# Performance work log

Measured on AMD Instinct MI355X. Metric: run time of the kernel, lower is better.

The kernel has to match this reference:

```python
import jax, jax.numpy as jnp
import numpy as np

B, S, T, D = 32, 128, 65536, 768
VOCAB, N_SEC, N_TEMP, N_NEG, MAX_SENT, N_TS = 30522, 6, 3, 2, 128, 512
LN_EPS = 1e-5


def setup_inputs() -> dict:
    key = jax.random.key(0)
    ks = jax.random.split(key, 16)
    return {
        "token_ids": jax.random.randint(ks[0], (T,), 0, VOCAB),
        "segment_ids": jnp.sort(jax.random.randint(ks[1], (T,), 0, B * S)),
        "section_ids": jax.random.randint(ks[2], (B, S), 0, N_SEC),
        "temporality_ids": jax.random.randint(ks[3], (B, S), 0, N_TEMP),
        "negation_ids": jax.random.randint(ks[4], (B, S), 0, N_NEG),
        "position_ids": jax.random.randint(ks[5], (B, S), 0, MAX_SENT),
        "timestamp_ids": jax.random.randint(ks[6], (B, S), 0, N_TS),
        "token_table": jax.random.normal(ks[7], (VOCAB, D), jnp.float32),
        "section_table": jax.random.normal(ks[8], (N_SEC, D), jnp.float32),
        "temporality_table": jax.random.normal(ks[9], (N_TEMP, D), jnp.float32),
        "negation_table": jax.random.normal(ks[10], (N_NEG, D), jnp.float32),
        "position_table": jax.random.normal(ks[11], (MAX_SENT, D), jnp.float32),
        "timestamp_table": jax.random.normal(ks[12], (N_TS, D), jnp.float32),
        "ln_gamma": jnp.ones((D,), jnp.float32),
        "ln_beta": jnp.zeros((D,), jnp.float32),
        "proj_w": jax.random.normal(ks[13], (D, D), jnp.float32) * (1.0 / np.sqrt(D)),
        "proj_b": jnp.zeros((D,), jnp.float32),
    }


def reference(token_ids, segment_ids, section_ids, temporality_ids, negation_ids,
              position_ids, timestamp_ids, token_table, section_table,
              temporality_table, negation_table, position_table, timestamp_table,
              ln_gamma, ln_beta, proj_w, proj_b):
    # ragged per-sentence token-embedding mean pool (segment mean over B*S slots)
    tok = token_table[token_ids]                                  # [T, D]
    sums = jax.ops.segment_sum(tok, segment_ids, num_segments=B * S)
    cnt = jax.ops.segment_sum(jnp.ones((T,), tok.dtype), segment_ids,
                              num_segments=B * S)
    base = (sums / jnp.maximum(cnt, 1.0)[:, None]).reshape(B, S, D)
    # multi-embedding sum
    enriched = (base
                + section_table[section_ids]
                + temporality_table[temporality_ids]
                + negation_table[negation_ids]
                + position_table[position_ids]
                + timestamp_table[timestamp_ids])                 # [B, S, D]
    # LayerNorm + Linear
    mu = enriched.mean(-1, keepdims=True)
    var = jnp.mean(jnp.square(enriched - mu), axis=-1, keepdims=True)
    normed = (enriched - mu) * jax.lax.rsqrt(var + LN_EPS) * ln_gamma + ln_beta
    tokens = jnp.einsum('bsd,ed->bse', normed, proj_w) + proj_b   # [B, S, D]
    padding_mask = jnp.zeros((B, S), dtype=bool)                  # all sentences valid
    return tokens, padding_mask
```

## Files before the change

### kernel.cpp

```cpp
#include <hip/hip_runtime.h>
#include <stdint.h>

#define Tn 65536
#define Dn 768
#define NSEG 4096

typedef __bf16 bf16;
typedef __bf16 bf16x8 __attribute__((ext_vector_type(8)));
typedef float f32x4 __attribute__((ext_vector_type(4)));

__device__ inline void f4add(float4& a, const float4& v) {
  a.x += v.x; a.y += v.y; a.z += v.z; a.w += v.w;
}

__device__ inline float block_sum192(float v, float* sm) {
  #pragma unroll
  for (int o = 32; o > 0; o >>= 1) v += __shfl_down(v, o, 64);
  const int lane = threadIdx.x & 63, w = threadIdx.x >> 6;
  __syncthreads();
  if (lane == 0) sm[w] = v;
  __syncthreads();
  return sm[0] + sm[1] + sm[2];
}

__global__ __launch_bounds__(192) void k_pool_ln(
    const int* __restrict__ token_ids, const int* __restrict__ segment_ids,
    const int* __restrict__ section_ids, const int* __restrict__ temporality_ids,
    const int* __restrict__ negation_ids, const int* __restrict__ position_ids,
    const int* __restrict__ timestamp_ids,
    const float* __restrict__ token_table, const float* __restrict__ section_table,
    const float* __restrict__ temporality_table, const float* __restrict__ negation_table,
    const float* __restrict__ position_table, const float* __restrict__ timestamp_table,
    const float* __restrict__ gamma, const float* __restrict__ beta,
    bf16* __restrict__ out_normed)
{
  const int n = blockIdx.x;
  const int tid = threadIdx.x;
  __shared__ float red[3];

  int lo = 0, hi = Tn;
  while (lo < hi) { int mid = (lo + hi) >> 1; if (segment_ids[mid] < n) lo = mid + 1; else hi = mid; }
  const int start = lo;
  hi = Tn;
  while (lo < hi) { int mid = (lo + hi) >> 1; if (segment_ids[mid] < n + 1) lo = mid + 1; else hi = mid; }
  const int end = lo;
  const float scale = 1.0f / fmaxf((float)(end - start), 1.0f);

  const int sec = section_ids[n];
  const int tmp = temporality_ids[n];
  const int neg = negation_ids[n];
  const int pos = position_ids[n];
  const int ts  = timestamp_ids[n];
  const float4 v1 = *(const float4*)(section_table     + (size_t)sec * Dn + 4 * tid);
  const float4 v2 = *(const float4*)(temporality_table + (size_t)tmp * Dn + 4 * tid);
  const float4 v3 = *(const float4*)(negation_table    + (size_t)neg * Dn + 4 * tid);
  const float4 v4 = *(const float4*)(position_table    + (size_t)pos * Dn + 4 * tid);
  const float4 v5 = *(const float4*)(timestamp_table   + (size_t)ts  * Dn + 4 * tid);

  const float4* tt = (const float4*)token_table;
  float4 a0 = make_float4(0.f,0.f,0.f,0.f), a1 = a0, a2 = a0, a3 = a0;
  int t = start;
  for (; t + 4 <= end; t += 4) {
    const int i0 = token_ids[t + 0];
    const int i1 = token_ids[t + 1];
    const int i2 = token_ids[t + 2];
    const int i3 = token_ids[t + 3];
    const float4 w0 = tt[(size_t)i0 * 192 + tid];
    const float4 w1 = tt[(size_t)i1 * 192 + tid];
    const float4 w2 = tt[(size_t)i2 * 192 + tid];
    const float4 w3 = tt[(size_t)i3 * 192 + tid];
    f4add(a0, w0); f4add(a1, w1); f4add(a2, w2); f4add(a3, w3);
  }
  for (; t < end; ++t) {
    const float4 w0 = tt[(size_t)token_ids[t] * 192 + tid];
    f4add(a0, w0);
  }
  f4add(a0, a1); f4add(a2, a3); f4add(a0, a2);

  float4 e;
  e.x = a0.x * scale + v1.x + v2.x + v3.x + v4.x + v5.x;
  e.y = a0.y * scale + v1.y + v2.y + v3.y + v4.y + v5.y;
  e.z = a0.z * scale + v1.z + v2.z + v3.z + v4.z + v5.z;
  e.w = a0.w * scale + v1.w + v2.w + v3.w + v4.w + v5.w;

  const float mu = block_sum192(e.x + e.y + e.z + e.w, red) * (1.0f / 768.0f);
  const float dx = e.x - mu, dy = e.y - mu, dz = e.z - mu, dw = e.w - mu;
  const float var = block_sum192(dx*dx + dy*dy + dz*dz + dw*dw, red) * (1.0f / 768.0f);
  const float inv = rsqrtf(var + 1e-5f);

  const float4 g = *(const float4*)(gamma + 4 * tid);
  const float4 b = *(const float4*)(beta  + 4 * tid);
  alignas(8) bf16 o[4];
  o[0] = (bf16)(dx * inv * g.x + b.x);
  o[1] = (bf16)(dy * inv * g.y + b.y);
  o[2] = (bf16)(dz * inv * g.z + b.z);
  o[3] = (bf16)(dw * inv * g.w + b.w);
  *(ushort4*)(out_normed + (size_t)n * Dn + 4 * tid) = *(ushort4*)o;
}

__global__ __launch_bounds__(256) void k_cvt_mask(const float* __restrict__ w,
                                                  bf16* __restrict__ wb,
                                                  float* __restrict__ mask_out) {
  const int b = blockIdx.x;
  if (b < 576) {
    const int i = b * 256 + threadIdx.x;
    const float4 v = ((const float4*)w)[i];
    alignas(8) bf16 o[4] = {(bf16)v.x, (bf16)v.y, (bf16)v.z, (bf16)v.w};
    ((ushort4*)wb)[i] = *(ushort4*)o;
  } else {
    mask_out[(b - 576) * 256 + threadIdx.x] = 0.0f;
  }
}

__global__ __launch_bounds__(256) void k_gemm(
    const bf16* __restrict__ A, const bf16* __restrict__ W,
    const float* __restrict__ bias, float* __restrict__ out)
{
  __shared__ bf16 As[64 * 32];
  __shared__ bf16 Bs[128 * 32];
  const int tid  = threadIdx.x;
  const int lane = tid & 63;
  const int w    = tid >> 6;
  const int m0 = blockIdx.y * 64;
  const int n0 = blockIdx.x * 128;
  const int wm = (w >> 1) * 32;
  const int wn = (w & 1) * 64;

  f32x4 acc[2][4];
  #pragma unroll
  for (int i = 0; i < 2; ++i)
    #pragma unroll
    for (int j = 0; j < 4; ++j) acc[i][j] = (f32x4){0.f, 0.f, 0.f, 0.f};

  const int fr = tid >> 2;
  const int fc = (tid & 3) * 8;
  const bf16* agp = A + (size_t)(m0 + fr) * 768 + fc;
  const bf16* bgp = W + (size_t)(n0 + fr) * 768 + fc;

  for (int kt = 0; kt < 24; ++kt) {
    __syncthreads();
    __builtin_amdgcn_global_load_lds(
        (const __attribute__((address_space(1))) void*)(agp + kt * 32),
        (__attribute__((address_space(3))) void*)(As + tid * 8), 16, 0, 0);
    #pragma unroll
    for (int it = 0; it < 2; ++it) {
      const int f = it * 256 + tid;
      __builtin_amdgcn_global_load_lds(
          (const __attribute__((address_space(1))) void*)(bgp + (size_t)it * 64 * 768 + kt * 32),
          (__attribute__((address_space(3))) void*)(Bs + f * 8), 16, 0, 0);
    }
    __syncthreads();

    bf16x8 af[2], bfr[4];
    #pragma unroll
    for (int i = 0; i < 2; ++i)
      af[i] = *(const bf16x8*)(As + (wm + i * 16 + (lane & 15)) * 32 + (lane >> 4) * 8);
    #pragma unroll
    for (int j = 0; j < 4; ++j)
      bfr[j] = *(const bf16x8*)(Bs + (wn + j * 16 + (lane & 15)) * 32 + (lane >> 4) * 8);

    #pragma unroll
    for (int i = 0; i < 2; ++i)
      #pragma unroll
      for (int j = 0; j < 4; ++j)
        acc[i][j] = __builtin_amdgcn_mfma_f32_16x16x32_bf16(af[i], bfr[j], acc[i][j], 0, 0, 0);
  }

  float bvals[4];
  #pragma unroll
  for (int j = 0; j < 4; ++j) bvals[j] = bias[n0 + wn + j * 16 + (lane & 15)];
  const int r0 = (lane >> 4) * 4;
  #pragma unroll
  for (int i = 0; i < 2; ++i) {
    #pragma unroll
    for (int r = 0; r < 4; ++r) {
      const int gm = m0 + wm + i * 16 + r0 + r;
      float* orow = out + (size_t)gm * 768 + n0 + wn;
      #pragma unroll
      for (int j = 0; j < 4; ++j)
        orow[j * 16 + (lane & 15)] = acc[i][j][r] + bvals[j];
    }
  }
}

extern "C" void kernel_launch(void* const* d_in, const int* in_sizes, int n_in,
                              void* d_out, int out_size, void* d_ws, size_t ws_size,
                              hipStream_t stream) {
  const int* token_ids       = (const int*)d_in[0];
  const int* segment_ids     = (const int*)d_in[1];
  const int* section_ids     = (const int*)d_in[2];
  const int* temporality_ids = (const int*)d_in[3];
  const int* negation_ids    = (const int*)d_in[4];
  const int* position_ids    = (const int*)d_in[5];
  const int* timestamp_ids   = (const int*)d_in[6];
  const float* token_table       = (const float*)d_in[7];
  const float* section_table     = (const float*)d_in[8];
  const float* temporality_table = (const float*)d_in[9];
  const float* negation_table    = (const float*)d_in[10];
  const float* position_table    = (const float*)d_in[11];
  const float* timestamp_table   = (const float*)d_in[12];
  const float* ln_gamma = (const float*)d_in[13];
  const float* ln_beta  = (const float*)d_in[14];
  const float* proj_w   = (const float*)d_in[15];
  const float* proj_b   = (const float*)d_in[16];

  float* out = (float*)d_out;
  bf16* wsW = (bf16*)d_ws;
  bf16* wsN = (bf16*)d_ws + (size_t)Dn * Dn;

  k_cvt_mask<<<592, 256, 0, stream>>>(proj_w, wsW, out + (size_t)NSEG * Dn);
  k_pool_ln<<<NSEG, 192, 0, stream>>>(token_ids, segment_ids, section_ids,
      temporality_ids, negation_ids, position_ids, timestamp_ids,
      token_table, section_table, temporality_table, negation_table,
      position_table, timestamp_table, ln_gamma, ln_beta, wsN);
  k_gemm<<<dim3(6, 64), 256, 0, stream>>>(wsN, wsW, proj_b, out);
}
```

Before: 209.3 us.

## Precompute segment starts and use one wave per segment for pooling+LayerNorm

```diff
diff --git a/kernel.cpp b/kernel.cpp
--- a/kernel.cpp
+++ b/kernel.cpp
@@ -13,18 +13,31 @@
   a.x += v.x; a.y += v.y; a.z += v.z; a.w += v.w;
 }
 
-__device__ inline float block_sum192(float v, float* sm) {
-  #pragma unroll
-  for (int o = 32; o > 0; o >>= 1) v += __shfl_down(v, o, 64);
-  const int lane = threadIdx.x & 63, w = threadIdx.x >> 6;
-  __syncthreads();
-  if (lane == 0) sm[w] = v;
-  __syncthreads();
-  return sm[0] + sm[1] + sm[2];
-}
-
-__global__ __launch_bounds__(192) void k_pool_ln(
-    const int* __restrict__ token_ids, const int* __restrict__ segment_ids,
+__global__ __launch_bounds__(256) void k_prep(
+    const float* __restrict__ w, bf16* __restrict__ wb,
+    float* __restrict__ mask_out,
+    const int* __restrict__ seg, int* __restrict__ starts)
+{
+  const int b = blockIdx.x;
+  if (b < 576) {
+    const int i = b * 256 + threadIdx.x;
+    const float4 v = ((const float4*)w)[i];
+    alignas(8) bf16 o[4] = {(bf16)v.x, (bf16)v.y, (bf16)v.z, (bf16)v.w};
+    ((ushort4*)wb)[i] = *(ushort4*)o;
+  } else if (b < 592) {
+    mask_out[(b - 576) * 256 + threadIdx.x] = 0.0f;
+  } else {
+    const int t = (b - 592) * 256 + threadIdx.x;
+    const int s = seg[t];
+    const int sp = (t == 0) ? -1 : seg[t - 1];
+    for (int k = sp + 1; k <= s; ++k) starts[k] = t;
+    if (t == Tn - 1)
+      for (int k = s + 1; k <= NSEG; ++k) starts[k] = Tn;
+  }
+}
+
+__global__ __launch_bounds__(64) void k_pool_ln(
+    const int* __restrict__ token_ids, const int* __restrict__ starts,
     const int* __restrict__ section_ids, const int* __restrict__ temporality_ids,
     const int* __restrict__ negation_ids, const int* __restrict__ position_ids,
     const int* __restrict__ timestamp_ids,
@@ -35,80 +48,95 @@
     bf16* __restrict__ out_normed)
 {
   const int n = blockIdx.x;
-  const int tid = threadIdx.x;
-  __shared__ float red[3];
-
-  int lo = 0, hi = Tn;
-  while (lo < hi) { int mid = (lo + hi) >> 1; if (segment_ids[mid] < n) lo = mid + 1; else hi = mid; }
-  const int start = lo;
-  hi = Tn;
-  while (lo < hi) { int mid = (lo + hi) >> 1; if (segment_ids[mid] < n + 1) lo = mid + 1; else hi = mid; }
-  const int end = lo;
+  const int lane = threadIdx.x;
+  const int start = starts[n];
+  const int end   = starts[n + 1];
   const float scale = 1.0f / fmaxf((float)(end - start), 1.0f);
 
-  const int sec = section_ids[n];
-  const int tmp = temporality_ids[n];
-  const int neg = negation_ids[n];
-  const int pos = position_ids[n];
-  const int ts  = timestamp_ids[n];
-  const float4 v1 = *(const float4*)(section_table     + (size_t)sec * Dn + 4 * tid);
-  const float4 v2 = *(const float4*)(temporality_table + (size_t)tmp * Dn + 4 * tid);
-  const float4 v3 = *(const float4*)(negation_table    + (size_t)neg * Dn + 4 * tid);
-  const float4 v4 = *(const float4*)(position_table    + (size_t)pos * Dn + 4 * tid);
-  const float4 v5 = *(const float4*)(timestamp_table   + (size_t)ts  * Dn + 4 * tid);
-
   const float4* tt = (const float4*)token_table;
-  float4 a0 = make_float4(0.f,0.f,0.f,0.f), a1 = a0, a2 = a0, a3 = a0;
+
+  const float4* e1 = (const float4*)(section_table     + (size_t)section_ids[n]     * Dn);
+  const float4* e2 = (const float4*)(temporality_table + (size_t)temporality_ids[n] * Dn);
+  const float4* e3 = (const float4*)(negation_table    + (size_t)negation_ids[n]    * Dn);
+  const float4* e4 = (const float4*)(position_table    + (size_t)position_ids[n]    * Dn);
+  const float4* e5 = (const float4*)(timestamp_table   + (size_t)timestamp_ids[n]   * Dn);
+  float4 en[3];
+  #pragma unroll
+  for (int j = 0; j < 3; ++j) {
+    const int d = j * 64 + lane;
+    float4 q = e1[d];
+    f4add(q, e2[d]); f4add(q, e3[d]); f4add(q, e4[d]); f4add(q, e5[d]);
+    en[j] = q;
+  }
+
+  float4 acc[3];
+  #pragma unroll
+  for (int j = 0; j < 3; ++j) acc[j] = make_float4(0.f, 0.f, 0.f, 0.f);
   int t = start;
   for (; t + 4 <= end; t += 4) {
     const int i0 = token_ids[t + 0];
     const int i1 = token_ids[t + 1];
     const int i2 = token_ids[t + 2];
     const int i3 = token_ids[t + 3];
-    const float4 w0 = tt[(size_t)i0 * 192 + tid];
-    const float4 w1 = tt[(size_t)i1 * 192 + tid];
-    const float4 w2 = tt[(size_t)i2 * 192 + tid];
-    const float4 w3 = tt[(size_t)i3 * 192 + tid];
-    f4add(a0, w0); f4add(a1, w1); f4add(a2, w2); f4add(a3, w3);
+    const float4* r0 = tt + (size_t)i0 * 192;
+    const float4* r1 = tt + (size_t)i1 * 192;
+    const float4* r2 = tt + (size_t)i2 * 192;
+    const float4* r3 = tt + (size_t)i3 * 192;
+    float4 L[4][3];
+    #pragma unroll
+    for (int j = 0; j < 3; ++j) {
+      const int d = j * 64 + lane;
+      L[0][j] = r0[d]; L[1][j] = r1[d]; L[2][j] = r2[d]; L[3][j] = r3[d];
+    }
+    #pragma unroll
+    for (int j = 0; j < 3; ++j) {
+      f4add(L[0][j], L[1][j]); f4add(L[2][j], L[3][j]);
+      f4add(L[0][j], L[2][j]); f4add(acc[j], L[0][j]);
+    }
   }
   for (; t < end; ++t) {
-    const float4 w0 = tt[(size_t)token_ids[t] * 192 + tid];
-    f4add(a0, w0);
-  }
-  f4add(a0, a1); f4add(a2, a3); f4add(a0, a2);
-
-  float4 e;
-  e.x = a0.x * scale + v1.x + v2.x + v3.x + v4.x + v5.x;
-  e.y = a0.y * scale + v1.y + v2.y + v3.y + v4.y + v5.y;
-  e.z = a0.z * scale + v1.z + v2.z + v3.z + v4.z + v5.z;
-  e.w = a0.w * scale + v1.w + v2.w + v3.w + v4.w + v5.w;
-
-  const float mu = block_sum192(e.x + e.y + e.z + e.w, red) * (1.0f / 768.0f);
-  const float dx = e.x - mu, dy = e.y - mu, dz = e.z - mu, dw = e.w - mu;
-  const float var = block_sum192(dx*dx + dy*dy + dz*dz + dw*dw, red) * (1.0f / 768.0f);
-  const float inv = rsqrtf(var + 1e-5f);
-
-  const float4 g = *(const float4*)(gamma + 4 * tid);
-  const float4 b = *(const float4*)(beta  + 4 * tid);
-  alignas(8) bf16 o[4];
-  o[0] = (bf16)(dx * inv * g.x + b.x);
-  o[1] = (bf16)(dy * inv * g.y + b.y);
-  o[2] = (bf16)(dz * inv * g.z + b.z);
-  o[3] = (bf16)(dw * inv * g.w + b.w);
-  *(ushort4*)(out_normed + (size_t)n * Dn + 4 * tid) = *(ushort4*)o;
-}
-
-__global__ __launch_bounds__(256) void k_cvt_mask(const float* __restrict__ w,
-                                                  bf16* __restrict__ wb,
-                                                  float* __restrict__ mask_out) {
-  const int b = blockIdx.x;
-  if (b < 576) {
-    const int i = b * 256 + threadIdx.x;
-    const float4 v = ((const float4*)w)[i];
-    alignas(8) bf16 o[4] = {(bf16)v.x, (bf16)v.y, (bf16)v.z, (bf16)v.w};
-    ((ushort4*)wb)[i] = *(ushort4*)o;
-  } else {
-    mask_out[(b - 576) * 256 + threadIdx.x] = 0.0f;
+    const float4* r = tt + (size_t)token_ids[t] * 192;
+    #pragma unroll
+    for (int j = 0; j < 3; ++j) f4add(acc[j], r[j * 64 + lane]);
+  }
+
+  float4 e[3];
+  #pragma unroll
+  for (int j = 0; j < 3; ++j) {
+    e[j].x = acc[j].x * scale + en[j].x;
+    e[j].y = acc[j].y * scale + en[j].y;
+    e[j].z = acc[j].z * scale + en[j].z;
+    e[j].w = acc[j].w * scale + en[j].w;
+  }
+
+  float s = 0.f;
+  #pragma unroll
+  for (int j = 0; j < 3; ++j) s += e[j].x + e[j].y + e[j].z + e[j].w;
+  #pragma unroll
+  for (int o = 32; o > 0; o >>= 1) s += __shfl_xor(s, o, 64);
+  const float mu = s * (1.0f / 768.0f);
+
+  float v = 0.f;
+  #pragma unroll
+  for (int j = 0; j < 3; ++j) {
+    e[j].x -= mu; e[j].y -= mu; e[j].z -= mu; e[j].w -= mu;
+    v += e[j].x * e[j].x + e[j].y * e[j].y + e[j].z * e[j].z + e[j].w * e[j].w;
+  }
+  #pragma unroll
+  for (int o = 32; o > 0; o >>= 1) v += __shfl_xor(v, o, 64);
+  const float inv = rsqrtf(v * (1.0f / 768.0f) + 1e-5f);
+
+  #pragma unroll
+  for (int j = 0; j < 3; ++j) {
+    const int d = j * 64 + lane;
+    const float4 g = ((const float4*)gamma)[d];
+    const float4 b = ((const float4*)beta)[d];
+    alignas(8) bf16 o[4];
+    o[0] = (bf16)(e[j].x * inv * g.x + b.x);
+    o[1] = (bf16)(e[j].y * inv * g.y + b.y);
+    o[2] = (bf16)(e[j].z * inv * g.z + b.z);
+    o[3] = (bf16)(e[j].w * inv * g.w + b.w);
+    *(ushort4*)(out_normed + (size_t)n * Dn + 4 * d) = *(ushort4*)o;
   }
 }
 
@@ -206,10 +234,12 @@
 
   float* out = (float*)d_out;
   bf16* wsW = (bf16*)d_ws;
-  bf16* wsN = (bf16*)d_ws + (size_t)Dn * Dn;
-
-  k_cvt_mask<<<592, 256, 0, stream>>>(proj_w, wsW, out + (size_t)NSEG * Dn);
-  k_pool_ln<<<NSEG, 192, 0, stream>>>(token_ids, segment_ids, section_ids,
+  bf16* wsN = wsW + (size_t)Dn * Dn;
+  int*  wsS = (int*)((char*)d_ws + (size_t)(Dn * Dn + NSEG * Dn) * 2);
+
+  k_prep<<<848, 256, 0, stream>>>(proj_w, wsW, out + (size_t)NSEG * Dn,
+                                  segment_ids, wsS);
+  k_pool_ln<<<NSEG, 64, 0, stream>>>(token_ids, wsS, section_ids,
       temporality_ids, negation_ids, position_ids, timestamp_ids,
       token_table, section_table, temporality_table, negation_table,
       position_table, timestamp_table, ln_gamma, ln_beta, wsN);
```

Measured after the change: 203.3 us. -2.9%, faster.
